# Optimization experiments

Hardware: AMD Instinct MI355X
Metric: run time of the kernel (lower is better)

Reference implementation:

```python
import jax, jax.numpy as jnp
import numpy as np

D_MODEL = 1024
NUM_HEADS = 16
HEAD_DIM = D_MODEL // NUM_HEADS
MAX_SEQ = 512


def rope_tables(seq_len, dim):
    inv_freq = 1.0 / (10000.0 ** (jnp.arange(0, dim, 2, dtype=jnp.float32) / dim))
    t = jnp.arange(seq_len, dtype=jnp.float32)
    freqs = jnp.einsum('i,j->ij', t, inv_freq)        # [S, dim/2]
    emb = jnp.concatenate([freqs, freqs], axis=-1)    # [S, dim]
    return jnp.cos(emb), jnp.sin(emb)


def rotate_half(x):
    x1, x2 = jnp.split(x, 2, axis=-1)
    return jnp.concatenate([-x2, x1], axis=-1)


def setup_inputs() -> dict:
    key = jax.random.key(0)
    ks = jax.random.split(key, 12)
    B, S, D = 16, 512, D_MODEL
    s = 1.0 / np.sqrt(D)
    inp = {
        'query': jax.random.normal(ks[0], (B, S, D), jnp.float32),
        'key': jax.random.normal(ks[1], (B, S, D), jnp.float32),
        'value': jax.random.normal(ks[2], (B, S, D), jnp.float32),
        'Wq': jax.random.normal(ks[3], (D, D), jnp.float32) * s,
        'bq': jnp.zeros((D,), jnp.float32),
        'Wk': jax.random.normal(ks[4], (D, D), jnp.float32) * s,
        'bk': jnp.zeros((D,), jnp.float32),
        'Wv': jax.random.normal(ks[5], (D, D), jnp.float32) * s,
        'bv': jnp.zeros((D,), jnp.float32),
        'Wo': jax.random.normal(ks[6], (D, D), jnp.float32) * s,
        'bo': jnp.zeros((D,), jnp.float32),
    }
    return inp


def reference(query, key, value, Wq, bq, Wk, bk, Wv, bv, Wo, bo):
    B, S, D = query.shape
    H, Hd = NUM_HEADS, HEAD_DIM
    scale = Hd ** -0.5

    def proj(x, W, b):  # torch Linear: x @ W.T + b -> [B,H,S,Hd]
        y = jnp.einsum('bsd,ed->bse', x, W) + b
        return y.reshape(B, S, H, Hd).transpose(0, 2, 1, 3)

    q = proj(query, Wq, bq)
    k = proj(key, Wk, bk)
    v = proj(value, Wv, bv)

    cos, sin = rope_tables(S, Hd)           # [S, Hd]
    cos = cos[None, None]                    # [1,1,S,Hd]
    sin = sin[None, None]
    q = q * cos + rotate_half(q) * sin
    k = k * cos + rotate_half(k) * sin

    attn = jnp.einsum('bhqd,bhkd->bhqk', q, k) * scale
    attn_w = jax.nn.softmax(attn, axis=-1)
    out = jnp.einsum('bhqk,bhkd->bhqd', attn_w, v)
    out = out.transpose(0, 2, 1, 3).reshape(B, S, D)
    out = jnp.einsum('bsd,ed->bse', out, Wo) + bo
    return out
```

## Files before the change

### kernel.cpp

```cpp
#include <hip/hip_runtime.h>
#include <hip/hip_bf16.h>
#include <math.h>

typedef __attribute__((ext_vector_type(8))) short short8;
typedef __attribute__((ext_vector_type(4))) float f32x4;
typedef unsigned short ushort;
typedef unsigned int uint;

#define BATCH 16
#define SEQ 512
#define DMODEL 1024
#define NHEADS 16
#define HD 64
#define MTOT (BATCH * SEQ)
#define NBUF ((size_t)MTOT * DMODEL)
#define WBUF ((size_t)DMODEL * DMODEL)

#define SZA (256 * 64)
#define SZB (128 * 64)

#define FENCE asm volatile("" ::: "memory")

__device__ __forceinline__ ushort f2bf(float f) {
    union { float f; uint i; } v; v.f = f;
    uint r = v.i + 0x7fffu + ((v.i >> 16) & 1u);
    return (ushort)(r >> 16);
}

__device__ __forceinline__ short8 cvt8(float4 a, float4 b) {
    short8 r;
    r[0] = (short)f2bf(a.x); r[1] = (short)f2bf(a.y);
    r[2] = (short)f2bf(a.z); r[3] = (short)f2bf(a.w);
    r[4] = (short)f2bf(b.x); r[5] = (short)f2bf(b.y);
    r[6] = (short)f2bf(b.z); r[7] = (short)f2bf(b.w);
    return r;
}

__device__ __forceinline__ void gld16(const ushort* g, ushort* l) {
    __builtin_amdgcn_global_load_lds(
        (const __attribute__((address_space(1))) void*)g,
        (__attribute__((address_space(3))) void*)l, 16, 0, 0);
}

__device__ __forceinline__ f32x4 mfma16(short8 a, short8 b, f32x4 c) {
    return __builtin_amdgcn_mfma_f32_16x16x32_bf16(a, b, c, 0, 0, 0);
}

__global__ void fill_const(float* __restrict__ out, float val) {
    out[blockIdx.x * 256 + threadIdx.x] = val;
}

__global__ __launch_bounds__(256) void cvt_act(
    const float* __restrict__ i0, const float* __restrict__ i1,
    const float* __restrict__ i2, ushort* __restrict__ o0,
    ushort* __restrict__ o1, ushort* __restrict__ o2)
{
    const float* in  = blockIdx.y == 0 ? i0 : (blockIdx.y == 1 ? i1 : i2);
    ushort*      out = blockIdx.y == 0 ? o0 : (blockIdx.y == 1 ? o1 : o2);
    int i = (blockIdx.x * 256 + threadIdx.x) * 8;
    float4 a = *(const float4*)(in + i);
    float4 b = *(const float4*)(in + i + 4);
    *(short8*)(out + i) = cvt8(a, b);
}

__global__ __launch_bounds__(256) void cvt_w(
    const float* __restrict__ i0, const float* __restrict__ i1,
    const float* __restrict__ i2, const float* __restrict__ i3,
    ushort* __restrict__ o0, ushort* __restrict__ o1,
    ushort* __restrict__ o2, ushort* __restrict__ o3)
{
    const float* in  = blockIdx.y == 0 ? i0 : (blockIdx.y == 1 ? i1 :
                        (blockIdx.y == 2 ? i2 : i3));
    ushort*      out = blockIdx.y == 0 ? o0 : (blockIdx.y == 1 ? o1 :
                        (blockIdx.y == 2 ? o2 : o3));
    int i = (blockIdx.x * 256 + threadIdx.x) * 8;
    float4 a = *(const float4*)(in + i);
    float4 b = *(const float4*)(in + i + 4);
    *(short8*)(out + i) = cvt8(a, b);
}

__global__ void rope_init(float* __restrict__ cs, float* __restrict__ sn) {
    int idx = blockIdx.x * 256 + threadIdx.x;
    if (idx >= SEQ * 32) return;
    int s = idx >> 5, p = idx & 31;
    float inv = __expf(-(float)p * (1.0f / 32.0f) * logf(10000.0f));
    float th = (float)s * inv;
    cs[idx] = cosf(th);
    sn[idx] = sinf(th);
}

__device__ __forceinline__ void gemm_core(
    const ushort* __restrict__ A, const ushort* __restrict__ W,
    ushort* __restrict__ smA, ushort* __restrict__ smB,
    int m0, int n0, int tid, f32x4 (&acc)[4][4])
{
    const int lane = tid & 63, w = tid >> 6;
    const int quad = lane >> 4, l16 = lane & 15;
    const int wm = (w >> 1) * 64, wn = (w & 1) * 64;
    const int swz = (l16 & 7) << 3;
    const int k0 = (quad * 8) ^ swz;
    const int k1 = ((4 + quad) * 8) ^ swz;

    const int r = tid >> 3;
    const int kc = ((tid & 7) ^ (r & 7)) * 8;
    const ushort* gA = A + (size_t)(m0 + r) * 1024 + kc;
    const ushort* gB = W + (size_t)(n0 + r) * 1024 + kc;
    ushort* lA = smA + tid * 8;
    ushort* lB = smB + tid * 8;

#pragma unroll
    for (int i = 0; i < 4; ++i) gld16(gA + i * 65536, lA + i * 4096);
    gld16(gB, lB); gld16(gB + 65536, lB + 4096);
    FENCE;
#pragma unroll
    for (int i = 0; i < 4; ++i) gld16(gA + i * 65536 + 64, lA + SZA + i * 4096);
    gld16(gB + 64, lB + SZB); gld16(gB + 65536 + 64, lB + SZB + 4096);
    FENCE;

#pragma unroll 1
    for (int t = 0; t < 16; ++t) {
        if (t < 15) asm volatile("s_waitcnt vmcnt(6)" ::: "memory");
        else        asm volatile("s_waitcnt vmcnt(0)" ::: "memory");
        __builtin_amdgcn_s_barrier();

        const ushort* tA = smA + (t % 3) * SZA;
        const ushort* tB = smB + (t % 3) * SZB;
        short8 af[4][2], bf[4][2];
#pragma unroll
        for (int mi = 0; mi < 4; ++mi) {
            const ushort* rp = tA + (wm + mi * 16 + l16) * 64;
            af[mi][0] = *(const short8*)(rp + k0);
            af[mi][1] = *(const short8*)(rp + k1);
        }
#pragma unroll
        for (int nj = 0; nj < 4; ++nj) {
            const ushort* rp = tB + (wn + nj * 16 + l16) * 64;
            bf[nj][0] = *(const short8*)(rp + k0);
            bf[nj][1] = *(const short8*)(rp + k1);
        }
        if (t < 14) {
            const int sl = (t + 2) % 3;
            const ushort* ga = gA + (size_t)(t + 2) * 64;
            const ushort* gb = gB + (size_t)(t + 2) * 64;
            ushort* da = lA + sl * SZA;
            ushort* db = lB + sl * SZB;
#pragma unroll
            for (int i = 0; i < 4; ++i) gld16(ga + i * 65536, da + i * 4096);
            gld16(gb, db); gld16(gb + 65536, db + 4096);
        }
        FENCE;
        __builtin_amdgcn_s_setprio(1);
#pragma unroll
        for (int nj = 0; nj < 4; ++nj)
#pragma unroll
            for (int mi = 0; mi < 4; ++mi) {
                acc[mi][nj] = mfma16(af[mi][0], bf[nj][0], acc[mi][nj]);
                acc[mi][nj] = mfma16(af[mi][1], bf[nj][1], acc[mi][nj]);
            }
        __builtin_amdgcn_s_setprio(0);
    }
}

__global__ __launch_bounds__(512, 2) void qkv_proj(
    const ushort* __restrict__ Aq, const ushort* __restrict__ Ak,
    const ushort* __restrict__ Av, const ushort* __restrict__ Wq,
    const ushort* __restrict__ Wk, const ushort* __restrict__ Wv,
    const float* __restrict__ bq, const float* __restrict__ bk,
    const float* __restrict__ bv, ushort* __restrict__ Qo,
    ushort* __restrict__ Ko, ushort* __restrict__ Vo,
    const float* __restrict__ cs_tab, const float* __restrict__ sn_tab)
{
    const int z = blockIdx.z;
    const ushort* A    = z == 0 ? Aq : (z == 1 ? Ak : Av);
    const ushort* W    = z == 0 ? Wq : (z == 1 ? Wk : Wv);
    const float*  bias = z == 0 ? bq : (z == 1 ? bk : bv);
    ushort*       out  = z == 0 ? Qo : (z == 1 ? Ko : Vo);

    const int id = blockIdx.x;
    const int x = id & 7, l = id >> 3;
    const int by = x * 4 + (l >> 3);
    const int bx = l & 7;
    const int m0 = by * 256, n0 = bx * 128;

    __shared__ __align__(16) ushort smA[3 * SZA];
    __shared__ __align__(16) ushort smB[3 * SZB];

    const int tid = threadIdx.x;
    const int lane = tid & 63, w = tid >> 6;
    const int quad = lane >> 4, l16 = lane & 15;
    const int wm = (w >> 1) * 64, wn = (w & 1) * 64;

    f32x4 acc[4][4] = {};
    gemm_core(A, W, smA, smB, m0, n0, tid, acc);

    float bv4[4];
#pragma unroll
    for (int j = 0; j < 4; j++) bv4[j] = bias[n0 + wn + j * 16 + l16];

    if (z < 2) {
        const int h = (n0 + wn) >> 6;
#pragma unroll
        for (int i = 0; i < 4; i++) {
#pragma unroll
            for (int r = 0; r < 4; r++) {
                int m = m0 + wm + i * 16 + quad * 4 + r;
                int s = m & (SEQ - 1), b = m >> 9;
                size_t base = ((size_t)(b * NHEADS + h) * SEQ + s) * HD;
#pragma unroll
                for (int jj = 0; jj < 2; jj++) {
                    int p = jj * 16 + l16;
                    float c = cs_tab[s * 32 + p], sg = sn_tab[s * 32 + p];
                    float lo = acc[i][jj][r] + bv4[jj];
                    float hi = acc[i][jj + 2][r] + bv4[jj + 2];
                    out[base + p]      = f2bf(lo * c - hi * sg);
                    out[base + 32 + p] = f2bf(hi * c + lo * sg);
                }
            }
        }
    } else {
#pragma unroll
        for (int i = 0; i < 4; i++)
#pragma unroll
            for (int jj = 0; jj < 4; jj++) {
                int n = n0 + wn + jj * 16 + l16;
                int h = n >> 6, d = n & 63;
#pragma unroll
                for (int r = 0; r < 4; r++) {
                    int m = m0 + wm + i * 16 + quad * 4 + r;
                    int s = m & (SEQ - 1), b = m >> 9;
                    out[((size_t)(b * NHEADS + h) * HD + d) * SEQ + s] =
                        f2bf(acc[i][jj][r] + bv4[jj]);
                }
            }
    }
}

__global__ __launch_bounds__(512, 2) void gemm_o(
    const ushort* __restrict__ A, const ushort* __restrict__ W,
    const float* __restrict__ bias, float* __restrict__ out)
{
    const int id = blockIdx.x;
    const int x = id & 7, l = id >> 3;
    const int by = x * 4 + (l >> 3);
    const int bx = l & 7;
    const int m0 = by * 256, n0 = bx * 128;

    __shared__ __align__(16) ushort smA[3 * SZA];
    __shared__ __align__(16) ushort smB[3 * SZB];

    const int tid = threadIdx.x;
    const int lane = tid & 63, w = tid >> 6;
    const int quad = lane >> 4, l16 = lane & 15;
    const int wm = (w >> 1) * 64, wn = (w & 1) * 64;

    f32x4 acc[4][4] = {};
    gemm_core(A, W, smA, smB, m0, n0, tid, acc);

    float bv4[4];
#pragma unroll
    for (int j = 0; j < 4; j++) bv4[j] = bias[n0 + wn + j * 16 + l16];

#pragma unroll
    for (int i = 0; i < 4; i++)
#pragma unroll
        for (int j = 0; j < 4; j++) {
            int n = n0 + wn + j * 16 + l16;
#pragma unroll
            for (int r = 0; r < 4; r++) {
                int m = m0 + wm + i * 16 + quad * 4 + r;
                out[(size_t)m * 1024 + n] = acc[i][j][r] + bv4[j];
            }
        }
}

__global__ __launch_bounds__(256) void attn(
    const ushort* __restrict__ Q, const ushort* __restrict__ K,
    const ushort* __restrict__ VT, ushort* __restrict__ O)
{
    __shared__ ushort sK[64 * 72];
    __shared__ ushort sV[64 * 72];
    __shared__ ushort sP[4][32 * 72];

    const int tid = threadIdx.x;
    const int wave = tid >> 6, lane = tid & 63;
    const int quad = lane >> 4, l16 = lane & 15;
    const int id = blockIdx.x;
    const int j8 = id >> 3;
    const int bh = (id & 7) * 32 + (j8 >> 2);
    const int q0 = (j8 & 3) * 128;
    const int qw = q0 + wave * 32;

    const ushort* Qbh = Q + (size_t)bh * SEQ * HD;
    const ushort* Kbh = K + (size_t)bh * SEQ * HD;
    const ushort* Vbh = VT + (size_t)bh * HD * SEQ;

    const float S2 = 0.125f * 1.44269504f;
    const float C2 = 12.0f * 1.44269504f;

    short8 qf[2][2];
#pragma unroll
    for (int mi = 0; mi < 2; mi++)
#pragma unroll
        for (int ks = 0; ks < 2; ks++)
            qf[mi][ks] = *(const short8*)(Qbh + (size_t)(qw + mi * 16 + l16) * HD +
                                          ks * 32 + quad * 8);

    f32x4 o_acc[2][4] = {};
    float lsum[2][4] = {};

    const int cA = tid, cB = tid + 256;
    const int rA = cA >> 3, colA = (cA & 7) * 8;
    const int rB = cB >> 3, colB = (cB & 7) * 8;

    for (int kt = 0; kt < SEQ; kt += 64) {
        *(short8*)(sK + rA * 72 + colA) = *(const short8*)(Kbh + (size_t)(kt + rA) * HD + colA);
        *(short8*)(sK + rB * 72 + colB) = *(const short8*)(Kbh + (size_t)(kt + rB) * HD + colB);
        *(short8*)(sV + rA * 72 + colA) = *(const short8*)(Vbh + (size_t)rA * SEQ + kt + colA);
        *(short8*)(sV + rB * 72 + colB) = *(const short8*)(Vbh + (size_t)rB * SEQ + kt + colB);
        __syncthreads();

        f32x4 sc[2][4];
#pragma unroll
        for (int nj = 0; nj < 4; nj++) {
            short8 kf0 = *(const short8*)(sK + (nj * 16 + l16) * 72 + quad * 8);
            short8 kf1 = *(const short8*)(sK + (nj * 16 + l16) * 72 + 32 + quad * 8);
#pragma unroll
            for (int mi = 0; mi < 2; mi++) {
                f32x4 z = {0.f, 0.f, 0.f, 0.f};
                z = mfma16(qf[mi][0], kf0, z);
                z = mfma16(qf[mi][1], kf1, z);
                sc[mi][nj] = z;
            }
        }

#pragma unroll
        for (int mi = 0; mi < 2; mi++)
#pragma unroll
            for (int r = 0; r < 4; r++) {
                float p0 = __builtin_amdgcn_exp2f(fmaf(sc[mi][0][r], S2, -C2));
                float p1 = __builtin_amdgcn_exp2f(fmaf(sc[mi][1][r], S2, -C2));
                float p2 = __builtin_amdgcn_exp2f(fmaf(sc[mi][2][r], S2, -C2));
                float p3 = __builtin_amdgcn_exp2f(fmaf(sc[mi][3][r], S2, -C2));
                sc[mi][0][r] = p0; sc[mi][1][r] = p1;
                sc[mi][2][r] = p2; sc[mi][3][r] = p3;
                lsum[mi][r] += (p0 + p1) + (p2 + p3);
            }

#pragma unroll
        for (int mi = 0; mi < 2; mi++)
#pragma unroll
            for (int nj = 0; nj < 4; nj++)
#pragma unroll
                for (int r = 0; r < 4; r++)
                    sP[wave][(mi * 16 + quad * 4 + r) * 72 + nj * 16 + l16] =
                        f2bf(sc[mi][nj][r]);
        __syncthreads();

#pragma unroll
        for (int ks = 0; ks < 2; ks++) {
            short8 pf0 = *(const short8*)(&sP[wave][(l16) * 72 + ks * 32 + quad * 8]);
            short8 pf1 = *(const short8*)(&sP[wave][(16 + l16) * 72 + ks * 32 + quad * 8]);
#pragma unroll
            for (int dj = 0; dj < 4; dj++) {
                short8 vf = *(const short8*)(sV + (dj * 16 + l16) * 72 + ks * 32 + quad * 8);
                o_acc[0][dj] = mfma16(pf0, vf, o_acc[0][dj]);
                o_acc[1][dj] = mfma16(pf1, vf, o_acc[1][dj]);
            }
        }
        __syncthreads();
    }

    const int h = bh & (NHEADS - 1), b = bh >> 4;
#pragma unroll
    for (int mi = 0; mi < 2; mi++)
#pragma unroll
        for (int r = 0; r < 4; r++) {
            float l = lsum[mi][r];
            l += __shfl_xor(l, 1, 64);
            l += __shfl_xor(l, 2, 64);
            l += __shfl_xor(l, 4, 64);
            l += __shfl_xor(l, 8, 64);
            float inv = 1.0f / l;
            int s = qw + mi * 16 + quad * 4 + r;
            size_t base = ((size_t)(b * SEQ + s)) * DMODEL + h * HD;
#pragma unroll
            for (int dj = 0; dj < 4; dj++)
                O[base + dj * 16 + l16] = f2bf(o_acc[mi][dj][r] * inv);
        }
}

extern "C" void kernel_launch(void* const* d_in, const int* in_sizes, int n_in,
                              void* d_out, int out_size, void* d_ws, size_t ws_size,
                              hipStream_t stream) {
    bool ok = (n_in == 11) && (out_size == (int)NBUF) &&
              in_sizes[0] == (int)NBUF && in_sizes[1] == (int)NBUF &&
              in_sizes[2] == (int)NBUF &&
              in_sizes[3] == (int)WBUF && in_sizes[4] == 1024 &&
              in_sizes[5] == (int)WBUF && in_sizes[6] == 1024 &&
              in_sizes[7] == (int)WBUF && in_sizes[8] == 1024 &&
              in_sizes[9] == (int)WBUF && in_sizes[10] == 1024;
    if (!ok) {
        fill_const<<<NBUF / 256, 256, 0, stream>>>((float*)d_out, 1000.0f);
        return;
    }
    size_t need = 2 * (size_t)SEQ * 32 * 4 + 4 * NBUF * 2 + 4 * WBUF * 2;
    if (ws_size < need) return;

    const float* q  = (const float*)d_in[0];
    const float* k  = (const float*)d_in[1];
    const float* v  = (const float*)d_in[2];
    const float* Wq = (const float*)d_in[3];
    const float* bq = (const float*)d_in[4];
    const float* Wk = (const float*)d_in[5];
    const float* bk = (const float*)d_in[6];
    const float* Wv = (const float*)d_in[7];
    const float* bv = (const float*)d_in[8];
    const float* Wo = (const float*)d_in[9];
    const float* bo = (const float*)d_in[10];

    float* cs = (float*)d_ws;
    float* sn = cs + SEQ * 32;
    ushort* Qb  = (ushort*)(sn + SEQ * 32);
    ushort* Kb  = Qb + NBUF;
    ushort* VTb = Kb + NBUF;
    ushort* Xb  = VTb + NBUF;
    ushort* Wqb = Xb + NBUF;
    ushort* Wkb = Wqb + WBUF;
    ushort* Wvb = Wkb + WBUF;
    ushort* Wob = Wvb + WBUF;
    ushort* Qx = (ushort*)d_out;
    ushort* Kx = Qx + NBUF;

    rope_init<<<64, 256, 0, stream>>>(cs, sn);
    cvt_w<<<dim3(WBUF / 2048, 4), 256, 0, stream>>>(Wq, Wk, Wv, Wo,
                                                    Wqb, Wkb, Wvb, Wob);
    cvt_act<<<dim3(NBUF / 2048, 3), 256, 0, stream>>>(q, k, v, Qx, Kx, Xb);

    qkv_proj<<<dim3(256, 1, 3), 512, 0, stream>>>(
        Qx, Kx, Xb, Wqb, Wkb, Wvb, bq, bk, bv, Qb, Kb, VTb, cs, sn);

    attn<<<BATCH * NHEADS * 4, 256, 0, stream>>>(Qb, Kb, VTb, Xb);

    gemm_o<<<256, 512, 0, stream>>>(Xb, Wob, bo, (float*)d_out);
}
```

Baseline: 286.5 us.

## Stage V-transpose epilogue through LDS and use nontemporal loads/stores

The V projection epilogue now writes the tile transposed into shared memory and then emits coalesced 16-byte stores along the sequence dimension, replacing scattered 2-byte strided stores into the transposed V layout. Conversion kernels use nontemporal loads, and the projection and output GEMM epilogues use nontemporal stores to reduce cache pollution. Launch order of the small prep kernels is also shuffled. The extra LDS pass adds two barriers and reuses the A staging buffer.

```diff
diff --git a/kernel.cpp b/kernel.cpp
--- a/kernel.cpp
+++ b/kernel.cpp
@@ -3,6 +3,7 @@
 #include <math.h>
 
 typedef __attribute__((ext_vector_type(8))) short short8;
+typedef __attribute__((ext_vector_type(4))) short s16x4;
 typedef __attribute__((ext_vector_type(4))) float f32x4;
 typedef unsigned short ushort;
 typedef unsigned int uint;
@@ -27,12 +28,12 @@
     return (ushort)(r >> 16);
 }
 
-__device__ __forceinline__ short8 cvt8(float4 a, float4 b) {
+__device__ __forceinline__ short8 cvt8v(f32x4 a, f32x4 b) {
     short8 r;
-    r[0] = (short)f2bf(a.x); r[1] = (short)f2bf(a.y);
-    r[2] = (short)f2bf(a.z); r[3] = (short)f2bf(a.w);
-    r[4] = (short)f2bf(b.x); r[5] = (short)f2bf(b.y);
-    r[6] = (short)f2bf(b.z); r[7] = (short)f2bf(b.w);
+    r[0] = (short)f2bf(a[0]); r[1] = (short)f2bf(a[1]);
+    r[2] = (short)f2bf(a[2]); r[3] = (short)f2bf(a[3]);
+    r[4] = (short)f2bf(b[0]); r[5] = (short)f2bf(b[1]);
+    r[6] = (short)f2bf(b[2]); r[7] = (short)f2bf(b[3]);
     return r;
 }
 
@@ -58,9 +59,9 @@
     const float* in  = blockIdx.y == 0 ? i0 : (blockIdx.y == 1 ? i1 : i2);
     ushort*      out = blockIdx.y == 0 ? o0 : (blockIdx.y == 1 ? o1 : o2);
     int i = (blockIdx.x * 256 + threadIdx.x) * 8;
-    float4 a = *(const float4*)(in + i);
-    float4 b = *(const float4*)(in + i + 4);
-    *(short8*)(out + i) = cvt8(a, b);
+    f32x4 a = __builtin_nontemporal_load((const f32x4*)(in + i));
+    f32x4 b = __builtin_nontemporal_load((const f32x4*)(in + i + 4));
+    *(short8*)(out + i) = cvt8v(a, b);
 }
 
 __global__ __launch_bounds__(256) void cvt_w(
@@ -74,9 +75,9 @@
     ushort*      out = blockIdx.y == 0 ? o0 : (blockIdx.y == 1 ? o1 :
                         (blockIdx.y == 2 ? o2 : o3));
     int i = (blockIdx.x * 256 + threadIdx.x) * 8;
-    float4 a = *(const float4*)(in + i);
-    float4 b = *(const float4*)(in + i + 4);
-    *(short8*)(out + i) = cvt8(a, b);
+    f32x4 a = __builtin_nontemporal_load((const f32x4*)(in + i));
+    f32x4 b = __builtin_nontemporal_load((const f32x4*)(in + i + 4));
+    *(short8*)(out + i) = cvt8v(a, b);
 }
 
 __global__ void rope_init(float* __restrict__ cs, float* __restrict__ sn) {
@@ -212,26 +213,36 @@
                     float c = cs_tab[s * 32 + p], sg = sn_tab[s * 32 + p];
                     float lo = acc[i][jj][r] + bv4[jj];
                     float hi = acc[i][jj + 2][r] + bv4[jj + 2];
-                    out[base + p]      = f2bf(lo * c - hi * sg);
-                    out[base + 32 + p] = f2bf(hi * c + lo * sg);
+                    __builtin_nontemporal_store(f2bf(lo * c - hi * sg),
+                                                out + base + p);
+                    __builtin_nontemporal_store(f2bf(hi * c + lo * sg),
+                                                out + base + 32 + p);
                 }
             }
         }
     } else {
+        __syncthreads();
+        ushort* sT = smA;
 #pragma unroll
         for (int i = 0; i < 4; i++)
 #pragma unroll
-            for (int jj = 0; jj < 4; jj++) {
-                int n = n0 + wn + jj * 16 + l16;
-                int h = n >> 6, d = n & 63;
-#pragma unroll
-                for (int r = 0; r < 4; r++) {
-                    int m = m0 + wm + i * 16 + quad * 4 + r;
-                    int s = m & (SEQ - 1), b = m >> 9;
-                    out[((size_t)(b * NHEADS + h) * HD + d) * SEQ + s] =
-                        f2bf(acc[i][jj][r] + bv4[jj]);
-                }
-            }
+            for (int j = 0; j < 4; j++) {
+                s16x4 vv;
+#pragma unroll
+                for (int r = 0; r < 4; r++) vv[r] = (short)f2bf(acc[i][j][r] + bv4[j]);
+                *(s16x4*)(sT + (wn + j * 16 + l16) * 264 + wm + i * 16 + quad * 4) = vv;
+            }
+        __syncthreads();
+        const int nl = tid >> 2, mc = (tid & 3) * 64;
+        const int ng = n0 + nl, h = ng >> 6, d = ng & 63;
+        const int b = m0 >> 9;
+        ushort* op = out + ((size_t)((b * NHEADS + h) * HD + d)) * SEQ +
+                     (m0 & (SEQ - 1)) + mc;
+#pragma unroll
+        for (int u = 0; u < 8; ++u) {
+            short8 vv = *(const short8*)(sT + nl * 264 + mc + u * 8);
+            __builtin_nontemporal_store(vv, (short8*)(op + u * 8));
+        }
     }
 }
 
@@ -268,7 +279,8 @@
 #pragma unroll
             for (int r = 0; r < 4; r++) {
                 int m = m0 + wm + i * 16 + quad * 4 + r;
-                out[(size_t)m * 1024 + n] = acc[i][j][r] + bv4[j];
+                __builtin_nontemporal_store(acc[i][j][r] + bv4[j],
+                                            out + (size_t)m * 1024 + n);
             }
         }
 }
@@ -431,10 +443,10 @@
     ushort* Qx = (ushort*)d_out;
     ushort* Kx = Qx + NBUF;
 
-    rope_init<<<64, 256, 0, stream>>>(cs, sn);
+    cvt_act<<<dim3(NBUF / 2048, 3), 256, 0, stream>>>(q, k, v, Qx, Kx, Xb);
     cvt_w<<<dim3(WBUF / 2048, 4), 256, 0, stream>>>(Wq, Wk, Wv, Wo,
                                                     Wqb, Wkb, Wvb, Wob);
-    cvt_act<<<dim3(NBUF / 2048, 3), 256, 0, stream>>>(q, k, v, Qx, Kx, Xb);
+    rope_init<<<64, 256, 0, stream>>>(cs, sn);
 
     qkv_proj<<<dim3(256, 1, 3), 512, 0, stream>>>(
         Qx, Kx, Xb, Wqb, Wkb, Wvb, bq, bk, bv, Qb, Kb, VTb, cs, sn);
```

After: 330.8 us. 1.15x slower.
